# Optimization experiments

Measured on AMD Instinct MI355X. Metric: run time of the kernel, lower is better.

The kernel has to match this reference:

```python
import jax, jax.numpy as jnp
import numpy as np

N_NODES = 50000
N_EDGES = 600000
N_GRAPHS = 128
D = 128
L = 3
OUT = 10
BN_EPS = 1e-5


def setup_inputs() -> dict:
    key = jax.random.key(0)
    ks = jax.random.split(key, 8)
    x = jax.random.normal(ks[0], (N_NODES, D), dtype=jnp.float32)
    edge_index = jax.random.randint(ks[1], (2, N_EDGES), 0, N_NODES, dtype=jnp.int64)
    batch = jnp.sort(jax.random.randint(ks[2], (N_NODES,), 0, N_GRAPHS, dtype=jnp.int64))
    s = 0.05
    return {
        "x": x,
        "edge_index": edge_index,
        "batch": batch,
        "convW1": jax.random.normal(ks[3], (L, D, D), dtype=jnp.float32) * s,
        "convb1": jnp.zeros((L, D), dtype=jnp.float32),
        "convg": jnp.ones((L, D), dtype=jnp.float32),
        "convbt": jnp.zeros((L, D), dtype=jnp.float32),
        "convW2": jax.random.normal(ks[4], (L, D, D), dtype=jnp.float32) * s,
        "convb2": jnp.zeros((L, D), dtype=jnp.float32),
        "mW1": jax.random.normal(ks[5], (D, D), dtype=jnp.float32) * s,
        "mb1": jnp.zeros((D,), dtype=jnp.float32),
        "mg": jnp.ones((D,), dtype=jnp.float32),
        "mbt": jnp.zeros((D,), dtype=jnp.float32),
        "mW2": jax.random.normal(ks[6], (D, OUT), dtype=jnp.float32) * s,
        "mb2": jnp.zeros((OUT,), dtype=jnp.float32),
    }


def _mlp(h, W1, b1, g, bt, W2, b2):
    # PyG MLP: Linear -> BatchNorm(eval: mean=0, var=1) -> ReLU -> Linear (plain last)
    inv = 1.0 / jnp.sqrt(1.0 + BN_EPS)
    h = h @ W1 + b1
    h = jnp.maximum(h * (inv * g) + bt, 0.0)
    return h @ W2 + b2


def reference(x, edge_index, batch, convW1, convb1, convg, convbt, convW2, convb2,
              mW1, mb1, mg, mbt, mW2, mb2):
    src, dst = edge_index[0], edge_index[1]
    for l in range(L):
        # GINConv (eps=0): nn(x + scatter-add of neighbor features)
        agg = jax.ops.segment_sum(x[src], dst, num_segments=N_NODES)  # [N, D]
        x = _mlp(x + agg, convW1[l], convb1[l], convg[l], convbt[l], convW2[l], convb2[l])
        x = jnp.maximum(x, 0.0)  # .relu() after conv
    pooled = jax.ops.segment_sum(x, batch, num_segments=N_GRAPHS)  # [G, D]
    return _mlp(pooled, mW1, mb1, mg, mbt, mW2, mb2)  # [G, OUT]
```

## Files before the change

### kernel.cpp

```cpp
#include <hip/hip_runtime.h>

#define N_NODES 50000
#define N_EDGES 600000
#define N_GRAPHS 128
#define DIM 128
#define NLAYERS 3
#define NOUT 10
#define ELLW 48
#define LSTRIDE 136
#define ZROW N_NODES

typedef unsigned short u16;
typedef unsigned int u32;
typedef __attribute__((ext_vector_type(8))) short bf16x8;
typedef __attribute__((ext_vector_type(4))) float f32x4;

__device__ __forceinline__ float bf2f(u16 v) {
    unsigned u = ((unsigned)v) << 16;
    return __builtin_bit_cast(float, u);
}
__device__ __forceinline__ u16 f2bf(float f) {
    unsigned u = __builtin_bit_cast(unsigned, f);
    u = u + 0x7fffu + ((u >> 16) & 1u);
    return (u16)(u >> 16);
}

__global__ void zero_small(int* __restrict__ deg, float* __restrict__ pooled) {
    int i = blockIdx.x * blockDim.x + threadIdx.x;
    if (i < N_NODES) deg[i] = 0;
    if (i < N_GRAPHS * DIM) pooled[i] = 0.f;
}

__global__ void prep_ell(int* __restrict__ deg, u16* __restrict__ ell,
                         const int* __restrict__ srcs, const int* __restrict__ dsts) {
    int i = blockIdx.x * blockDim.x + threadIdx.x;
    if (i >= N_EDGES) return;
    int d = dsts[i];
    int slot = atomicAdd(&deg[d], 1);
    if (slot < ELLW) ell[(size_t)d * ELLW + slot] = (u16)srcs[i];
}

__global__ void prep_cvt(u16* __restrict__ xb, u16* __restrict__ bufA, u16* __restrict__ bufB,
                         const float* __restrict__ x, u16* __restrict__ Wswz,
                         const float* __restrict__ convW1, const float* __restrict__ convW2) {
    int i = blockIdx.x * blockDim.x + threadIdx.x;
    if (i < DIM) {
        xb[(size_t)ZROW * DIM + i] = 0;
        bufA[(size_t)ZROW * DIM + i] = 0;
        bufB[(size_t)ZROW * DIM + i] = 0;
    }
    if (i < 6 * 16384) {
        int j = i & 7, lane = (i >> 3) & 63, cb = (i >> 9) & 7, kc = (i >> 12) & 3, w = i >> 14;
        int k = kc * 32 + ((lane >> 4) << 3) + j;
        int c = (cb << 4) + (lane & 15);
        const float* W = (w < 3) ? (convW1 + (size_t)w * 16384) : (convW2 + (size_t)(w - 3) * 16384);
        Wswz[i] = f2bf(W[k * DIM + c]);
    }
    if (i < N_NODES * DIM / 4) {
        float4 v = ((const float4*)x)[i];
        ushort4 o;
        o.x = f2bf(v.x); o.y = f2bf(v.y); o.z = f2bf(v.z); o.w = f2bf(v.w);
        ((ushort4*)xb)[i] = o;
    }
}

template <int POOL>
__global__ __launch_bounds__(256) void layer_fused(
    u16* __restrict__ out, const u16* __restrict__ x,
    const int* __restrict__ deg, const u16* __restrict__ ell,
    const u16* __restrict__ W1f, const u16* __restrict__ W2f,
    const float* __restrict__ b1, const float* __restrict__ g1,
    const float* __restrict__ bt1, const float* __restrict__ b2,
    const int* __restrict__ batch, float* __restrict__ pooled) {
    __shared__ u16 A[16 * LSTRIDE];
    __shared__ u16 H[16 * LSTRIDE];
    __shared__ int gb[16];
    const int tid = threadIdx.x;
    const int wv = tid >> 6;
    const int lane = tid & 63;
    const int row0 = blockIdx.x * 16;

    if (POOL && tid < 16) gb[tid] = batch[row0 + tid];

    const size_t coff = (size_t)lane * 2;
    {
        const int r0 = wv << 2;
        int len[4];
        const u16* ep[4];
        float ax[4], ay[4];
#pragma unroll
        for (int r = 0; r < 4; ++r) {
            const int grow = row0 + r0 + r;
            len[r] = min(deg[grow], ELLW);
            ep[r] = ell + (size_t)grow * ELLW;
            ushort2 self = *(const ushort2*)(x + (size_t)grow * DIM + coff);
            ax[r] = bf2f(self.x);
            ay[r] = bf2f(self.y);
        }
        const int maxlen = max(max(len[0], len[1]), max(len[2], len[3]));
        for (int j = 0; j < maxlen; j += 8) {
            int id[4][8];
#pragma unroll
            for (int r = 0; r < 4; ++r) {
                uint4 e = *(const uint4*)(ep[r] + j);
                id[r][0] = (j + 0 < len[r]) ? (int)(e.x & 0xFFFFu) : ZROW;
                id[r][1] = (j + 1 < len[r]) ? (int)(e.x >> 16)     : ZROW;
                id[r][2] = (j + 2 < len[r]) ? (int)(e.y & 0xFFFFu) : ZROW;
                id[r][3] = (j + 3 < len[r]) ? (int)(e.y >> 16)     : ZROW;
                id[r][4] = (j + 4 < len[r]) ? (int)(e.z & 0xFFFFu) : ZROW;
                id[r][5] = (j + 5 < len[r]) ? (int)(e.z >> 16)     : ZROW;
                id[r][6] = (j + 6 < len[r]) ? (int)(e.w & 0xFFFFu) : ZROW;
                id[r][7] = (j + 7 < len[r]) ? (int)(e.w >> 16)     : ZROW;
            }
#pragma unroll
            for (int r = 0; r < 4; ++r) {
                float px = 0.f, py = 0.f;
#pragma unroll
                for (int t = 0; t < 8; ++t) {
                    ushort2 v = *(const ushort2*)(x + (size_t)id[r][t] * DIM + coff);
                    px += bf2f(v.x);
                    py += bf2f(v.y);
                }
                ax[r] += px;
                ay[r] += py;
            }
        }
#pragma unroll
        for (int r = 0; r < 4; ++r) {
            ushort2 o;
            o.x = f2bf(ax[r]);
            o.y = f2bf(ay[r]);
            *(ushort2*)&A[(r0 + r) * LSTRIDE + lane * 2] = o;
        }
    }
    __syncthreads();

    const float inv = rsqrtf(1.f + 1e-5f);
    const int col0 = lane & 15;
    const int rbl = (lane >> 4) << 2;
    const int fragoff = (lane & 15) * LSTRIDE + ((lane >> 4) << 3);

    {
        f32x4 acc[2];
        acc[0] = (f32x4){0.f, 0.f, 0.f, 0.f};
        acc[1] = (f32x4){0.f, 0.f, 0.f, 0.f};
#pragma unroll
        for (int kc = 0; kc < 4; ++kc) {
            bf16x8 a = *(const bf16x8*)&A[fragoff + kc * 32];
#pragma unroll
            for (int m = 0; m < 2; ++m) {
                const int cb = (wv << 1) + m;
                bf16x8 bb = *(const bf16x8*)(W1f + ((((kc << 3) + cb) << 6 | lane) << 3));
                acc[m] = __builtin_amdgcn_mfma_f32_16x16x32_bf16(a, bb, acc[m], 0, 0, 0);
            }
        }
#pragma unroll
        for (int m = 0; m < 2; ++m) {
            const int c = (((wv << 1) + m) << 4) + col0;
            const float bias = b1[c];
            const float sg = inv * g1[c];
            const float st = bt1[c];
#pragma unroll
            for (int q = 0; q < 4; ++q) {
                float v = (acc[m][q] + bias) * sg + st;
                H[(rbl + q) * LSTRIDE + c] = f2bf(fmaxf(v, 0.f));
            }
        }
    }
    __syncthreads();

    {
        f32x4 acc[2];
        acc[0] = (f32x4){0.f, 0.f, 0.f, 0.f};
        acc[1] = (f32x4){0.f, 0.f, 0.f, 0.f};
#pragma unroll
        for (int kc = 0; kc < 4; ++kc) {
            bf16x8 a = *(const bf16x8*)&H[fragoff + kc * 32];
#pragma unroll
            for (int m = 0; m < 2; ++m) {
                const int cb = (wv << 1) + m;
                bf16x8 bb = *(const bf16x8*)(W2f + ((((kc << 3) + cb) << 6 | lane) << 3));
                acc[m] = __builtin_amdgcn_mfma_f32_16x16x32_bf16(a, bb, acc[m], 0, 0, 0);
            }
        }
#pragma unroll
        for (int m = 0; m < 2; ++m) {
            const int c = (((wv << 1) + m) << 4) + col0;
            const float bias = b2[c];
#pragma unroll
            for (int q = 0; q < 4; ++q) {
                float v = acc[m][q] + bias;
                A[(rbl + q) * LSTRIDE + c] = f2bf(fmaxf(v, 0.f));
            }
        }
    }
    __syncthreads();

    if (!POOL) {
        const int r = tid >> 4;
        const int seg = tid & 15;
        uint4 v = *(const uint4*)&A[r * LSTRIDE + seg * 8];
        *(uint4*)(out + (size_t)(row0 + r) * DIM + seg * 8) = v;
    } else {
        const int c = tid & 127;
        const int rbeg = (tid >> 7) << 3;
        float acc = 0.f;
        int curg = gb[rbeg];
#pragma unroll
        for (int r = 0; r < 8; ++r) {
            const int g = gb[rbeg + r];
            if (g != curg) {
                atomicAdd(&pooled[(size_t)curg * DIM + c], acc);
                acc = 0.f;
                curg = g;
            }
            acc += bf2f(A[(rbeg + r) * LSTRIDE + c]);
        }
        atomicAdd(&pooled[(size_t)curg * DIM + c], acc);
    }
}

__global__ __launch_bounds__(128) void tail_mlp(float* __restrict__ out,
                                                const float* __restrict__ pooled,
                                                const float* __restrict__ mW1,
                                                const float* __restrict__ mb1,
                                                const float* __restrict__ mg,
                                                const float* __restrict__ mbt,
                                                const float* __restrict__ mW2,
                                                const float* __restrict__ mb2) {
    const int g = blockIdx.x;
    const int c = threadIdx.x;
    __shared__ float pl[DIM];
    __shared__ float hd[DIM];
    pl[c] = pooled[(size_t)g * DIM + c];
    __syncthreads();

    float s = 0.f;
#pragma unroll 4
    for (int k = 0; k < DIM; ++k) s += pl[k] * mW1[k * DIM + c];
    const float inv = rsqrtf(1.f + 1e-5f);
    s = (s + mb1[c]) * (inv * mg[c]) + mbt[c];
    hd[c] = fmaxf(s, 0.f);
    __syncthreads();

    if (c < NOUT) {
        float o = 0.f;
#pragma unroll 4
        for (int k = 0; k < DIM; ++k) o += hd[k] * mW2[k * NOUT + c];
        out[g * NOUT + c] = o + mb2[c];
    }
}

extern "C" void kernel_launch(void* const* d_in, const int* in_sizes, int n_in,
                              void* d_out, int out_size, void* d_ws, size_t ws_size,
                              hipStream_t stream) {
    const float* x      = (const float*)d_in[0];
    const int*   ei     = (const int*)d_in[1];
    const int*   batch  = (const int*)d_in[2];
    const float* convW1 = (const float*)d_in[3];
    const float* convb1 = (const float*)d_in[4];
    const float* convg  = (const float*)d_in[5];
    const float* convbt = (const float*)d_in[6];
    const float* convW2 = (const float*)d_in[7];
    const float* convb2 = (const float*)d_in[8];
    const float* mW1    = (const float*)d_in[9];
    const float* mb1    = (const float*)d_in[10];
    const float* mg     = (const float*)d_in[11];
    const float* mbt    = (const float*)d_in[12];
    const float* mW2    = (const float*)d_in[13];
    const float* mb2    = (const float*)d_in[14];
    float* out = (float*)d_out;

    const int* srcs = ei;
    const int* dsts = ei + N_EDGES;

    const size_t NFP = (size_t)(N_NODES + 1) * DIM;
    u16* xb0  = (u16*)d_ws;
    u16* bufA = xb0 + NFP;
    u16* bufB = bufA + NFP;
    u16* Wswz = bufB + NFP;
    float* pooled = (float*)(Wswz + 6 * 16384);
    int* deg = (int*)(pooled + N_GRAPHS * DIM);
    u16* ell = (u16*)(deg + N_NODES);

    zero_small<<<(N_NODES + 255) / 256, 256, 0, stream>>>(deg, pooled);
    prep_ell<<<(N_EDGES + 255) / 256, 256, 0, stream>>>(deg, ell, srcs, dsts);
    prep_cvt<<<(N_NODES * DIM / 4 + 255) / 256, 256, 0, stream>>>(
        xb0, bufA, bufB, x, Wswz, convW1, convW2);

    const int layerBlocks = N_NODES / 16;
    layer_fused<0><<<layerBlocks, 256, 0, stream>>>(
        bufA, xb0, deg, ell, Wswz, Wswz + (size_t)3 * 16384,
        convb1, convg, convbt, convb2, batch, pooled);
    layer_fused<0><<<layerBlocks, 256, 0, stream>>>(
        bufB, bufA, deg, ell, Wswz + (size_t)1 * 16384, Wswz + (size_t)4 * 16384,
        convb1 + DIM, convg + DIM, convbt + DIM, convb2 + DIM, batch, pooled);
    layer_fused<1><<<layerBlocks, 256, 0, stream>>>(
        bufA , bufB, deg, ell, Wswz + (size_t)2 * 16384, Wswz + (size_t)5 * 16384,
        convb1 + 2 * DIM, convg + 2 * DIM, convbt + 2 * DIM, convb2 + 2 * DIM, batch, pooled);

    tail_mlp<<<N_GRAPHS, 128, 0, stream>>>(out, pooled, mW1, mb1, mg, mbt, mW2, mb2);
}
```

Baseline: 155.8 us.

## Split fused layer into XCD-aware column-group gather and per-wave MLP kernels

Each fused layer kernel becomes two kernels. The first is a gather kernel that maps blocks to XCDs so each XCD's L2 only caches one quarter of the feature columns. The second is an MLP kernel where each wave computes all 128 output columns for its own 16 rows, with no block-level syncs. The aim is better L2 hit rates for the random neighbour gathers and less synchronisation in the GEMM phase. The cost is an extra aggregate buffer round trip through global memory and two launches per layer.

New measurement: 232.9 us. 1.49x slower.

```diff
diff --git a/kernel.cpp b/kernel.cpp
--- a/kernel.cpp
+++ b/kernel.cpp
@@ -9,6 +9,8 @@
 #define ELLW 48
 #define LSTRIDE 136
 #define ZROW N_NODES
+#define GTILE 64
+#define NGTILES 782
 
 typedef unsigned short u16;
 typedef unsigned int u32;
@@ -27,7 +29,7 @@
 
 __global__ void zero_small(int* __restrict__ deg, float* __restrict__ pooled) {
     int i = blockIdx.x * blockDim.x + threadIdx.x;
-    if (i < N_NODES) deg[i] = 0;
+    if (i < N_NODES + 64) deg[i] = 0;
     if (i < N_GRAPHS * DIM) pooled[i] = 0.f;
 }
 
@@ -64,76 +66,63 @@
     }
 }
 
+__global__ __launch_bounds__(256) void gather_cg(u16* __restrict__ agg,
+                                                 const u16* __restrict__ x,
+                                                 const int* __restrict__ deg,
+                                                 const u16* __restrict__ ell) {
+    const int b = blockIdx.x;
+    const int xcd = b & 7;
+    const int cg = xcd & 3;
+    const int tile = ((b >> 3) << 1) + (xcd >> 2);
+    const int row0 = tile * GTILE;
+    const int tid = threadIdx.x;
+    const int wv = tid >> 6;
+    const int lane = tid & 63;
+    const int rsub = lane >> 4;
+    const int coff = (cg << 5) + ((lane & 15) << 1);
+
+#pragma unroll
+    for (int g = 0; g < 4; ++g) {
+        const int row = row0 + (wv << 4) + (g << 2) + rsub;
+        const int grow = min(row, ZROW);
+        const int len = min(deg[grow], ELLW);
+        const u16* ep = ell + (size_t)grow * ELLW;
+        ushort2 self = *(const ushort2*)(x + (size_t)grow * DIM + coff);
+        float ax = bf2f(self.x), ay = bf2f(self.y);
+        for (int j = 0; __any(j < len); j += 4) {
+            ushort4 e = *(const ushort4*)(ep + j);
+            int i0 = (j + 0 < len) ? (int)e.x : ZROW;
+            int i1 = (j + 1 < len) ? (int)e.y : ZROW;
+            int i2 = (j + 2 < len) ? (int)e.z : ZROW;
+            int i3 = (j + 3 < len) ? (int)e.w : ZROW;
+            ushort2 v0 = *(const ushort2*)(x + (size_t)i0 * DIM + coff);
+            ushort2 v1 = *(const ushort2*)(x + (size_t)i1 * DIM + coff);
+            ushort2 v2 = *(const ushort2*)(x + (size_t)i2 * DIM + coff);
+            ushort2 v3 = *(const ushort2*)(x + (size_t)i3 * DIM + coff);
+            ax += (bf2f(v0.x) + bf2f(v1.x)) + (bf2f(v2.x) + bf2f(v3.x));
+            ay += (bf2f(v0.y) + bf2f(v1.y)) + (bf2f(v2.y) + bf2f(v3.y));
+        }
+        if (row < N_NODES) {
+            ushort2 o;
+            o.x = f2bf(ax);
+            o.y = f2bf(ay);
+            *(ushort2*)(agg + (size_t)row * DIM + coff) = o;
+        }
+    }
+}
+
 template <int POOL>
-__global__ __launch_bounds__(256) void layer_fused(
-    u16* __restrict__ out, const u16* __restrict__ x,
-    const int* __restrict__ deg, const u16* __restrict__ ell,
+__global__ __launch_bounds__(256) void mlp_pool(
+    u16* __restrict__ out, const u16* __restrict__ agg,
     const u16* __restrict__ W1f, const u16* __restrict__ W2f,
     const float* __restrict__ b1, const float* __restrict__ g1,
     const float* __restrict__ bt1, const float* __restrict__ b2,
     const int* __restrict__ batch, float* __restrict__ pooled) {
-    __shared__ u16 A[16 * LSTRIDE];
-    __shared__ u16 H[16 * LSTRIDE];
-    __shared__ int gb[16];
-    const int tid = threadIdx.x;
-    const int wv = tid >> 6;
-    const int lane = tid & 63;
-    const int row0 = blockIdx.x * 16;
-
-    if (POOL && tid < 16) gb[tid] = batch[row0 + tid];
-
-    const size_t coff = (size_t)lane * 2;
-    {
-        const int r0 = wv << 2;
-        int len[4];
-        const u16* ep[4];
-        float ax[4], ay[4];
-#pragma unroll
-        for (int r = 0; r < 4; ++r) {
-            const int grow = row0 + r0 + r;
-            len[r] = min(deg[grow], ELLW);
-            ep[r] = ell + (size_t)grow * ELLW;
-            ushort2 self = *(const ushort2*)(x + (size_t)grow * DIM + coff);
-            ax[r] = bf2f(self.x);
-            ay[r] = bf2f(self.y);
-        }
-        const int maxlen = max(max(len[0], len[1]), max(len[2], len[3]));
-        for (int j = 0; j < maxlen; j += 8) {
-            int id[4][8];
-#pragma unroll
-            for (int r = 0; r < 4; ++r) {
-                uint4 e = *(const uint4*)(ep[r] + j);
-                id[r][0] = (j + 0 < len[r]) ? (int)(e.x & 0xFFFFu) : ZROW;
-                id[r][1] = (j + 1 < len[r]) ? (int)(e.x >> 16)     : ZROW;
-                id[r][2] = (j + 2 < len[r]) ? (int)(e.y & 0xFFFFu) : ZROW;
-                id[r][3] = (j + 3 < len[r]) ? (int)(e.y >> 16)     : ZROW;
-                id[r][4] = (j + 4 < len[r]) ? (int)(e.z & 0xFFFFu) : ZROW;
-                id[r][5] = (j + 5 < len[r]) ? (int)(e.z >> 16)     : ZROW;
-                id[r][6] = (j + 6 < len[r]) ? (int)(e.w & 0xFFFFu) : ZROW;
-                id[r][7] = (j + 7 < len[r]) ? (int)(e.w >> 16)     : ZROW;
-            }
-#pragma unroll
-            for (int r = 0; r < 4; ++r) {
-                float px = 0.f, py = 0.f;
-#pragma unroll
-                for (int t = 0; t < 8; ++t) {
-                    ushort2 v = *(const ushort2*)(x + (size_t)id[r][t] * DIM + coff);
-                    px += bf2f(v.x);
-                    py += bf2f(v.y);
-                }
-                ax[r] += px;
-                ay[r] += py;
-            }
-        }
-#pragma unroll
-        for (int r = 0; r < 4; ++r) {
-            ushort2 o;
-            o.x = f2bf(ax[r]);
-            o.y = f2bf(ay[r]);
-            *(ushort2*)&A[(r0 + r) * LSTRIDE + lane * 2] = o;
-        }
-    }
-    __syncthreads();
+    __shared__ u16 lds[4][16 * LSTRIDE];
+    const int wv = threadIdx.x >> 6;
+    const int lane = threadIdx.x & 63;
+    const int row0 = blockIdx.x * 64 + wv * 16;
+    u16* H = lds[wv];
 
     const float inv = rsqrtf(1.f + 1e-5f);
     const int col0 = lane & 15;
@@ -141,82 +130,87 @@
     const int fragoff = (lane & 15) * LSTRIDE + ((lane >> 4) << 3);
 
     {
-        f32x4 acc[2];
-        acc[0] = (f32x4){0.f, 0.f, 0.f, 0.f};
-        acc[1] = (f32x4){0.f, 0.f, 0.f, 0.f};
+        const int arow = min(row0 + (lane & 15), N_NODES - 1);
+        const u16* ap = agg + (size_t)arow * DIM + ((lane >> 4) << 3);
+        f32x4 acc[8];
+#pragma unroll
+        for (int cb = 0; cb < 8; ++cb) acc[cb] = (f32x4){0.f, 0.f, 0.f, 0.f};
 #pragma unroll
         for (int kc = 0; kc < 4; ++kc) {
-            bf16x8 a = *(const bf16x8*)&A[fragoff + kc * 32];
-#pragma unroll
-            for (int m = 0; m < 2; ++m) {
-                const int cb = (wv << 1) + m;
+            bf16x8 a = *(const bf16x8*)(ap + kc * 32);
+#pragma unroll
+            for (int cb = 0; cb < 8; ++cb) {
                 bf16x8 bb = *(const bf16x8*)(W1f + ((((kc << 3) + cb) << 6 | lane) << 3));
-                acc[m] = __builtin_amdgcn_mfma_f32_16x16x32_bf16(a, bb, acc[m], 0, 0, 0);
-            }
-        }
-#pragma unroll
-        for (int m = 0; m < 2; ++m) {
-            const int c = (((wv << 1) + m) << 4) + col0;
+                acc[cb] = __builtin_amdgcn_mfma_f32_16x16x32_bf16(a, bb, acc[cb], 0, 0, 0);
+            }
+        }
+#pragma unroll
+        for (int cb = 0; cb < 8; ++cb) {
+            const int c = (cb << 4) + col0;
             const float bias = b1[c];
             const float sg = inv * g1[c];
             const float st = bt1[c];
 #pragma unroll
             for (int q = 0; q < 4; ++q) {
-                float v = (acc[m][q] + bias) * sg + st;
+                float v = (acc[cb][q] + bias) * sg + st;
                 H[(rbl + q) * LSTRIDE + c] = f2bf(fmaxf(v, 0.f));
             }
         }
     }
-    __syncthreads();
 
     {
-        f32x4 acc[2];
-        acc[0] = (f32x4){0.f, 0.f, 0.f, 0.f};
-        acc[1] = (f32x4){0.f, 0.f, 0.f, 0.f};
+        f32x4 acc[8];
+#pragma unroll
+        for (int cb = 0; cb < 8; ++cb) acc[cb] = (f32x4){0.f, 0.f, 0.f, 0.f};
 #pragma unroll
         for (int kc = 0; kc < 4; ++kc) {
             bf16x8 a = *(const bf16x8*)&H[fragoff + kc * 32];
 #pragma unroll
-            for (int m = 0; m < 2; ++m) {
-                const int cb = (wv << 1) + m;
+            for (int cb = 0; cb < 8; ++cb) {
                 bf16x8 bb = *(const bf16x8*)(W2f + ((((kc << 3) + cb) << 6 | lane) << 3));
-                acc[m] = __builtin_amdgcn_mfma_f32_16x16x32_bf16(a, bb, acc[m], 0, 0, 0);
-            }
-        }
-#pragma unroll
-        for (int m = 0; m < 2; ++m) {
-            const int c = (((wv << 1) + m) << 4) + col0;
+                acc[cb] = __builtin_amdgcn_mfma_f32_16x16x32_bf16(a, bb, acc[cb], 0, 0, 0);
+            }
+        }
+#pragma unroll
+        for (int cb = 0; cb < 8; ++cb) {
+            const int c = (cb << 4) + col0;
             const float bias = b2[c];
 #pragma unroll
             for (int q = 0; q < 4; ++q) {
-                float v = acc[m][q] + bias;
-                A[(rbl + q) * LSTRIDE + c] = f2bf(fmaxf(v, 0.f));
-            }
-        }
-    }
-    __syncthreads();
+                float v = acc[cb][q] + bias;
+                H[(rbl + q) * LSTRIDE + c] = f2bf(fmaxf(v, 0.f));
+            }
+        }
+    }
 
     if (!POOL) {
-        const int r = tid >> 4;
-        const int seg = tid & 15;
-        uint4 v = *(const uint4*)&A[r * LSTRIDE + seg * 8];
-        *(uint4*)(out + (size_t)(row0 + r) * DIM + seg * 8) = v;
+#pragma unroll
+        for (int it = 0; it < 8; ++it) {
+            const int r = it * 2 + (lane >> 5);
+            const int grow = row0 + r;
+            const int m = lane & 31;
+            uint2 v = *(const uint2*)&H[r * LSTRIDE + m * 4];
+            if (grow < N_NODES) *(uint2*)(out + (size_t)grow * DIM + m * 4) = v;
+        }
     } else {
-        const int c = tid & 127;
-        const int rbeg = (tid >> 7) << 3;
-        float acc = 0.f;
-        int curg = gb[rbeg];
-#pragma unroll
-        for (int r = 0; r < 8; ++r) {
-            const int g = gb[rbeg + r];
+        const int c0 = lane * 2;
+        float sx = 0.f, sy = 0.f;
+        int curg = batch[min(row0, N_NODES - 1)];
+        for (int r = 0; r < 16; ++r) {
+            const int row = row0 + r;
+            const int g = batch[min(row, N_NODES - 1)];
             if (g != curg) {
-                atomicAdd(&pooled[(size_t)curg * DIM + c], acc);
-                acc = 0.f;
-                curg = g;
-            }
-            acc += bf2f(A[(rbeg + r) * LSTRIDE + c]);
-        }
-        atomicAdd(&pooled[(size_t)curg * DIM + c], acc);
+                atomicAdd(&pooled[(size_t)curg * DIM + c0], sx);
+                atomicAdd(&pooled[(size_t)curg * DIM + c0 + 1], sy);
+                sx = 0.f; sy = 0.f; curg = g;
+            }
+            if (row < N_NODES) {
+                sx += bf2f(H[r * LSTRIDE + c0]);
+                sy += bf2f(H[r * LSTRIDE + c0 + 1]);
+            }
+        }
+        atomicAdd(&pooled[(size_t)curg * DIM + c0], sx);
+        atomicAdd(&pooled[(size_t)curg * DIM + c0 + 1], sy);
     }
 }
 
@@ -278,26 +272,37 @@
     u16* xb0  = (u16*)d_ws;
     u16* bufA = xb0 + NFP;
     u16* bufB = bufA + NFP;
-    u16* Wswz = bufB + NFP;
+    u16* aggbuf = bufB + NFP;
+    u16* Wswz = aggbuf + (size_t)N_NODES * DIM;
     float* pooled = (float*)(Wswz + 6 * 16384);
     int* deg = (int*)(pooled + N_GRAPHS * DIM);
-    u16* ell = (u16*)(deg + N_NODES);
-
-    zero_small<<<(N_NODES + 255) / 256, 256, 0, stream>>>(deg, pooled);
+    u16* ell = (u16*)(deg + N_NODES + 64);
+
+    zero_small<<<(N_NODES + 64 + 255) / 256, 256, 0, stream>>>(deg, pooled);
     prep_ell<<<(N_EDGES + 255) / 256, 256, 0, stream>>>(deg, ell, srcs, dsts);
     prep_cvt<<<(N_NODES * DIM / 4 + 255) / 256, 256, 0, stream>>>(
         xb0, bufA, bufB, x, Wswz, convW1, convW2);
 
-    const int layerBlocks = N_NODES / 16;
-    layer_fused<0><<<layerBlocks, 256, 0, stream>>>(
-        bufA, xb0, deg, ell, Wswz, Wswz + (size_t)3 * 16384,
-        convb1, convg, convbt, convb2, batch, pooled);
-    layer_fused<0><<<layerBlocks, 256, 0, stream>>>(
-        bufB, bufA, deg, ell, Wswz + (size_t)1 * 16384, Wswz + (size_t)4 * 16384,
-        convb1 + DIM, convg + DIM, convbt + DIM, convb2 + DIM, batch, pooled);
-    layer_fused<1><<<layerBlocks, 256, 0, stream>>>(
-        bufA , bufB, deg, ell, Wswz + (size_t)2 * 16384, Wswz + (size_t)5 * 16384,
-        convb1 + 2 * DIM, convg + 2 * DIM, convbt + 2 * DIM, convb2 + 2 * DIM, batch, pooled);
+    const int gatherBlocks = (NGTILES / 2) * 8;
+    const int mlpBlocks    = (N_NODES + 63) / 64;
+    const u16* cur = xb0;
+    u16* nxt = bufA;
+    for (int l = 0; l < NLAYERS; ++l) {
+        gather_cg<<<gatherBlocks, 256, 0, stream>>>(aggbuf, cur, deg, ell);
+        if (l < NLAYERS - 1) {
+            mlp_pool<0><<<mlpBlocks, 256, 0, stream>>>(
+                nxt, aggbuf, Wswz + (size_t)l * 16384, Wswz + (size_t)(3 + l) * 16384,
+                convb1 + l * DIM, convg + l * DIM, convbt + l * DIM, convb2 + l * DIM,
+                batch, pooled);
+        } else {
+            mlp_pool<1><<<mlpBlocks, 256, 0, stream>>>(
+                nxt, aggbuf, Wswz + (size_t)l * 16384, Wswz + (size_t)(3 + l) * 16384,
+                convb1 + l * DIM, convg + l * DIM, convbt + l * DIM, convb2 + l * DIM,
+                batch, pooled);
+        }
+        cur = nxt;
+        nxt = (nxt == bufA) ? bufB : bufA;
+    }
 
     tail_mlp<<<N_GRAPHS, 128, 0, stream>>>(out, pooled, mW1, mb1, mg, mbt, mW2, mb2);
 }
```
